# Kernel optimization log

Measured on AMD Instinct MI355X. Metric: run time of the kernel, lower is better.

The kernel has to match this reference:

```python
import jax, jax.numpy as jnp
import numpy as np

PAD = 1
VOCAB, D, HOPS = 32000, 256, 3

def _gru_dir(x_tbd, h0, Wih, Whh, bih, bhh):
    # x_tbd: [T,B,D]; PyTorch GRU gate math
    def step(h, xt):
        gx = xt @ Wih.T + bih            # [B,3D]
        gh = h @ Whh.T + bhh
        xr, xz, xn = jnp.split(gx, 3, axis=-1)
        hr, hz, hn = jnp.split(gh, 3, axis=-1)
        r = jax.nn.sigmoid(xr + hr)
        z = jax.nn.sigmoid(xz + hz)
        n = jnp.tanh(xn + r * hn)
        h2 = (1.0 - z) * n + z * h
        return h2, h2
    hT, ys = jax.lax.scan(step, h0, x_tbd)
    return ys, hT

def _embed_bag(table, idx):
    # idx: [B,L,M] -> sum over M -> [B,L,D]
    return jnp.take(table, idx, axis=0).sum(axis=2)

def _add_lm(full_mem, kb_len, conv_len, hiddens):
    # full_mem: [B,L,D]; hiddens: [B,T,D]; write hiddens into rows [kb, kb+cl)
    B, L, _ = full_mem.shape
    T = hiddens.shape[1]
    pos = jnp.arange(L)[None, :]                      # [1,L]
    rel = pos - kb_len[:, None]                        # [B,L]
    valid = (rel >= 0) & (rel < conv_len[:, None])
    rel_c = jnp.clip(rel, 0, T - 1)
    gathered = jnp.take_along_axis(hiddens, rel_c[:, :, None], axis=1)  # [B,L,D]
    return full_mem + jnp.where(valid[:, :, None], gathered, 0.0)

def setup_inputs() -> dict:
    key = jax.random.key(0)
    ks = jax.random.split(key, 20)
    B, T, L, M = 32, 128, 512, 4
    conv_seqs = jax.random.randint(ks[0], (B, T, M), 0, VOCAB)
    src_seqs = jax.random.randint(ks[1], (B, L, M), 0, VOCAB)
    kb_len = jnp.full((B,), L - T, dtype=jnp.int32)
    conv_len = jnp.full((B,), T, dtype=jnp.int32)
    def zero_pad(t):
        return t.at[PAD].set(0.0)
    emb_ctx = zero_pad(0.1 * jax.random.normal(ks[2], (VOCAB, D)))
    C_tables = zero_pad(0.1 * jax.random.normal(ks[3], (HOPS + 1, VOCAB, D)).transpose(1, 0, 2)).transpose(1, 0, 2)
    s = 1.0 / np.sqrt(D)
    Wih_f = jax.random.uniform(ks[4], (3 * D, D), minval=-s, maxval=s)
    Whh_f = jax.random.uniform(ks[5], (3 * D, D), minval=-s, maxval=s)
    bih_f = jax.random.uniform(ks[6], (3 * D,), minval=-s, maxval=s)
    bhh_f = jax.random.uniform(ks[7], (3 * D,), minval=-s, maxval=s)
    Wih_b = jax.random.uniform(ks[8], (3 * D, D), minval=-s, maxval=s)
    Whh_b = jax.random.uniform(ks[9], (3 * D, D), minval=-s, maxval=s)
    bih_b = jax.random.uniform(ks[10], (3 * D,), minval=-s, maxval=s)
    bhh_b = jax.random.uniform(ks[11], (3 * D,), minval=-s, maxval=s)
    W_w = jax.random.uniform(ks[12], (D, 2 * D), minval=-s, maxval=s)
    W_b = jax.random.uniform(ks[13], (D,), minval=-s, maxval=s)
    proj_w = jax.random.uniform(ks[14], (D, 2 * D), minval=-s, maxval=s)
    proj_b = jax.random.uniform(ks[15], (D,), minval=-s, maxval=s)
    return dict(conv_seqs=conv_seqs, src_seqs=src_seqs, kb_len=kb_len, conv_len=conv_len,
                emb_ctx=emb_ctx, C_tables=C_tables,
                Wih_f=Wih_f, Whh_f=Whh_f, bih_f=bih_f, bhh_f=bhh_f,
                Wih_b=Wih_b, Whh_b=Whh_b, bih_b=bih_b, bhh_b=bhh_b,
                W_w=W_w, W_b=W_b, proj_w=proj_w, proj_b=proj_b)

def reference(conv_seqs, src_seqs, kb_len, conv_len, emb_ctx, C_tables,
              Wih_f, Whh_f, bih_f, bhh_f, Wih_b, Whh_b, bih_b, bhh_b,
              W_w, W_b, proj_w, proj_b):
    B = conv_seqs.shape[0]
    # ContextRNN (dropout is identity at eval)
    emb = _embed_bag(emb_ctx, conv_seqs)               # [B,T,D]
    x = emb.transpose(1, 0, 2)                          # [T,B,D]
    h0 = jnp.zeros((B, D), emb.dtype)
    ys_f, hT_f = _gru_dir(x, h0, Wih_f, Whh_f, bih_f, bhh_f)
    ys_b, hT_b = _gru_dir(x[::-1], h0, Wih_b, Whh_b, bih_b, bhh_b)
    outputs = jnp.concatenate([ys_f, ys_b[::-1]], axis=-1).transpose(1, 0, 2)  # [B,T,2D]
    hidden = jnp.concatenate([hT_f, hT_b], axis=-1) @ W_w.T + W_b              # [B,D]
    rnn_out = outputs @ W_w.T + W_b                                            # [B,T,D]
    # ExternalKnowledge encode
    u = hidden
    prob_logit = None
    embed_C = None
    for hop in range(HOPS):
        embed_A = _add_lm(_embed_bag(C_tables[hop], src_seqs), kb_len, conv_len, rnn_out)
        embed_C = _add_lm(_embed_bag(C_tables[hop + 1], src_seqs), kb_len, conv_len, rnn_out)
        prob_logit = jnp.einsum('bld,bd->bl', embed_A, u)
        prob = jax.nn.softmax(prob_logit, axis=1)
        o_k = jnp.einsum('bld,bl->bd', embed_C, prob)
        u = u + o_k
    global_pointer = jax.nn.sigmoid(prob_logit)
    encoded = jax.nn.relu(jnp.concatenate([hidden, u], axis=-1) @ proj_w.T + proj_b)[None]
    return global_pointer, encoded
```

## Files before the change

### kernel.cpp

```cpp
#include <hip/hip_runtime.h>

typedef _Float16 f16;
typedef _Float16 f16x8 __attribute__((ext_vector_type(8)));
typedef _Float16 f16x4 __attribute__((ext_vector_type(4)));
typedef float    f32x4 __attribute__((ext_vector_type(4)));


__device__ __forceinline__ float frcp(float x){
  float r; asm("v_rcp_f32 %0, %1" : "=v"(r) : "v"(x)); return r;
}
__device__ __forceinline__ float fsig(float x){ return frcp(1.0f + __expf(-x)); }
__device__ __forceinline__ float ftanh(float x){ return 2.0f*frcp(1.0f + __expf(-2.0f*x)) - 1.0f; }

__global__ void k_zero(float* out){
  int i = blockIdx.x*256 + threadIdx.x;
  if (i < 24576) out[i] = 0.f;
}

__global__ void k_cvtall(const float* __restrict__ s0, const float* __restrict__ s1,
                         const float* __restrict__ s2, const float* __restrict__ s3,
                         const float* __restrict__ s4,
                         f16* __restrict__ d0, f16* __restrict__ d1,
                         f16* __restrict__ d2, f16* __restrict__ d3,
                         f16* __restrict__ d4){
  int i = blockIdx.x*256 + threadIdx.x;
  d0[i] = (f16)s0[i];
  d1[i] = (f16)s1[i];
  d2[i] = (f16)s2[i];
  d3[i] = (f16)s3[i];
  if (i < 131072) d4[i] = (f16)s4[i];
}

__global__ void k_embbag(const int* __restrict__ conv, const float* __restrict__ tbl,
                         f16* __restrict__ emb){
  int bt = blockIdx.x, d = threadIdx.x;
  const int* ix = conv + (size_t)bt*4;
  float s = 0.f;
#pragma unroll
  for (int m = 0; m < 4; ++m) s += tbl[(size_t)ix[m]*256 + d];
  emb[(size_t)bt*256 + d] = (f16)s;
}

__global__ __launch_bounds__(256) void k_gx(const f16* __restrict__ emb,
                                            const f16* __restrict__ W16,
                                            const float* __restrict__ bih,
                                            const float* __restrict__ bhh,
                                            f16* __restrict__ gx, int rev){
  int lane = threadIdx.x & 63, wv = threadIdx.x >> 6;
  int l16 = lane & 15, l4 = lane >> 4;
  int mrow = blockIdx.x*64 + wv*16;
  int m = mrow + l16;
  int t = m >> 5, b = m & 31;
  int tsrc = rev ? (127 - t) : t;
  const f16* arow = emb + (size_t)(b*128 + tsrc)*256;
  f16x8 af[8];
#pragma unroll
  for (int kt = 0; kt < 8; ++kt) af[kt] = *(const f16x8*)(arow + kt*32 + l4*8);

  for (int nt = 0; nt < 48; ++nt){
    int n = nt*16 + l16;
    const f16* brow = W16 + (size_t)n*256;
    f32x4 acc = {0.f,0.f,0.f,0.f};
#pragma unroll
    for (int kt = 0; kt < 8; ++kt){
      f16x8 bf = *(const f16x8*)(brow + kt*32 + l4*8);
      acc = __builtin_amdgcn_mfma_f32_16x16x32_f16(af[kt], bf, acc, 0, 0, 0);
    }
    float bias = bih[n] + (n < 512 ? bhh[n] : 0.f);
#pragma unroll
    for (int r = 0; r < 4; ++r){
      int m2 = mrow + l4*4 + r;
      gx[(size_t)m2*768 + n] = (f16)(acc[r] + bias);
    }
  }
}

__global__ __launch_bounds__(512, 1) void k_gru(const f16* __restrict__ gx_f,
                                                const f16* __restrict__ gx_b,
                                                const f16* __restrict__ whhf16,
                                                const f16* __restrict__ whhb16,
                                                const float* __restrict__ bhh_f,
                                                const float* __restrict__ bhh_b,
                                                f16* __restrict__ Abuf){
  int dir = blockIdx.x >> 1, grp = blockIdx.x & 1, b0 = grp*16;
  const f16*   gx  = dir ? gx_b   : gx_f;
  const f16*   Whh = dir ? whhb16 : whhf16;
  const float* bhh = dir ? bhh_b  : bhh_f;

  int tid = threadIdx.x, lane = tid & 63, wv = tid >> 6;
  int l16 = lane & 15, l4 = lane >> 4;

  __shared__ __align__(16) f16   a16[2][16][264];
  __shared__ __align__(16) float bhnL[256];
  for (int i = tid; i < (16*264*2)/4; i += 512) ((unsigned*)&a16[0][0][0])[i] = 0u;
  if (tid < 256) bhnL[tid] = bhh[512 + tid];

  f16x8 aW[2][3][8];
#pragma unroll
  for (int q = 0; q < 2; ++q){
    int Q = 2*wv + q;
#pragma unroll
    for (int g = 0; g < 3; ++g){
      const f16* wrow = Whh + (size_t)(g*256 + Q*16 + l16)*256;
#pragma unroll
      for (int kt = 0; kt < 8; ++kt) aW[q][g][kt] = *(const f16x8*)(wrow + kt*32 + l4*8);
    }
  }

  const f16* gp = gx + (size_t)(b0 + l16)*768;
  f16* ap  = Abuf + (size_t)(b0 + l16)*128*512 + dir*256 + (size_t)(dir ? 127 : 0)*512;
  int  astep = dir ? -512 : 512;
  f16* app = ap;

  const int d00 = (2*wv    )*16 + l4*4;
  const int d01 = (2*wv + 1)*16 + l4*4;

  f16x4 pend[2];
  pend[0] = (f16x4){(f16)0.f,(f16)0.f,(f16)0.f,(f16)0.f};
  pend[1] = (f16x4){(f16)0.f,(f16)0.f,(f16)0.f,(f16)0.f};

  __syncthreads();

#pragma unroll 1
  for (int t = 0; t < 128; ++t){
    if (t){
      *(f16x4*)(app + d00) = pend[0];
      *(f16x4*)(app + d01) = pend[1];
    }
    f16x4 xg[2][3];
#pragma unroll
    for (int q = 0; q < 2; ++q)
#pragma unroll
      for (int g = 0; g < 3; ++g)
        xg[q][g] = *(const f16x4*)(gp + g*256 + (2*wv+q)*16 + l4*4);

    const f16* rb = &a16[t & 1][l16][l4*8];

    f32x4 accr[2], accz[2];
#pragma unroll
    for (int q = 0; q < 2; ++q){ accr[q] = (f32x4){0.f,0.f,0.f,0.f};
                                 accz[q] = (f32x4){0.f,0.f,0.f,0.f}; }
#pragma unroll
    for (int kt = 0; kt < 8; ++kt){
      f16x8 bf = *(const f16x8*)(rb + kt*32);
#pragma unroll
      for (int q = 0; q < 2; ++q){
        accr[q] = __builtin_amdgcn_mfma_f32_16x16x32_f16(aW[q][0][kt], bf, accr[q], 0, 0, 0);
        accz[q] = __builtin_amdgcn_mfma_f32_16x16x32_f16(aW[q][1][kt], bf, accz[q], 0, 0, 0);
      }
    }
    f32x4 accn[2];
#pragma unroll
    for (int q = 0; q < 2; ++q) accn[q] = (f32x4){0.f,0.f,0.f,0.f};
#pragma unroll
    for (int kt = 0; kt < 8; ++kt){
      f16x8 bf = *(const f16x8*)(rb + kt*32);
#pragma unroll
      for (int q = 0; q < 2; ++q)
        accn[q] = __builtin_amdgcn_mfma_f32_16x16x32_f16(aW[q][2][kt], bf, accn[q], 0, 0, 0);
    }
    float rr[2][4], zz[2][4];
#pragma unroll
    for (int q = 0; q < 2; ++q)
#pragma unroll
      for (int r = 0; r < 4; ++r){
        rr[q][r] = fsig((float)xg[q][0][r] + accr[q][r]);
        zz[q][r] = fsig((float)xg[q][1][r] + accz[q][r]);
      }
    int nxt = (t & 1) ^ 1;
#pragma unroll
    for (int q = 0; q < 2; ++q){
      int d0 = (2*wv+q)*16 + l4*4;
      float4 bh4 = *(const float4*)(&bhnL[d0]);
      f16x4 hold = pend[q];
      f16x4 o4;
#pragma unroll
      for (int r = 0; r < 4; ++r){
        float bh = (r==0)?bh4.x:(r==1)?bh4.y:(r==2)?bh4.z:bh4.w;
        float nn = ftanh((float)xg[q][2][r] + rr[q][r]*(accn[q][r] + bh));
        float h2 = nn + zz[q][r]*((float)hold[r] - nn);
        o4[r] = (f16)h2;
      }
      *(f16x4*)(&a16[nxt][l16][d0]) = o4;
      pend[q] = o4;
    }
    app = ap; ap += astep;
    gp += 24576;
    __syncthreads();
  }
  *(f16x4*)(app + d00) = pend[0];
  *(f16x4*)(app + d01) = pend[1];
}

__global__ __launch_bounds__(256) void k_rnnout(const f16* __restrict__ Abuf,
                                                const f16* __restrict__ Ww16,
                                                const float* __restrict__ Wb,
                                                float* __restrict__ rnn){
  int lane = threadIdx.x & 63, wv = threadIdx.x >> 6;
  int l16 = lane & 15, l4 = lane >> 4;
  int mrow = blockIdx.x*64 + wv*16;
  const f16* arow = Abuf + (size_t)(mrow + l16)*512;
  f16x8 af[16];
#pragma unroll
  for (int kt = 0; kt < 16; ++kt) af[kt] = *(const f16x8*)(arow + kt*32 + l4*8);
  for (int nt = 0; nt < 16; ++nt){
    int n = nt*16 + l16;
    const f16* brow = Ww16 + (size_t)n*512;
    f32x4 acc = {0.f,0.f,0.f,0.f};
#pragma unroll
    for (int kt = 0; kt < 16; ++kt){
      f16x8 bf = *(const f16x8*)(brow + kt*32 + l4*8);
      acc = __builtin_amdgcn_mfma_f32_16x16x32_f16(af[kt], bf, acc, 0, 0, 0);
    }
    float bias = Wb[n];
#pragma unroll
    for (int r = 0; r < 4; ++r)
      rnn[(size_t)(mrow + l4*4 + r)*256 + n] = acc[r] + bias;
  }
}

__global__ __launch_bounds__(256) void k_hidden(const f16* __restrict__ Abuf,
                                                const f16* __restrict__ Ww16,
                                                const float* __restrict__ Wb,
                                                float* __restrict__ hidden,
                                                float* __restrict__ u){
  int lane = threadIdx.x & 63, wv = threadIdx.x >> 6;
  int l16 = lane & 15, l4 = lane >> 4;
  int mt = wv & 1, nt = blockIdx.x*2 + (wv >> 1);
  int b = mt*16 + l16;
  const f16* rowf = Abuf + ((size_t)b*128 + 127)*512;
  const f16* rowb = Abuf + ((size_t)b*128)*512;
  f16x8 af[16];
#pragma unroll
  for (int kt = 0; kt < 16; ++kt){
    int k = kt*32 + l4*8;
    af[kt] = *(const f16x8*)((k < 256 ? rowf : rowb) + k);
  }
  int n = nt*16 + l16;
  const f16* brow = Ww16 + (size_t)n*512;
  f32x4 acc = {0.f,0.f,0.f,0.f};
#pragma unroll
  for (int kt = 0; kt < 16; ++kt){
    f16x8 bf = *(const f16x8*)(brow + kt*32 + l4*8);
    acc = __builtin_amdgcn_mfma_f32_16x16x32_f16(af[kt], bf, acc, 0, 0, 0);
  }
  float bias = Wb[n];
#pragma unroll
  for (int r = 0; r < 4; ++r){
    int bo = mt*16 + l4*4 + r;
    float v = acc[r] + bias;
    hidden[(size_t)bo*256 + n] = v;
    u[(size_t)bo*256 + n] = v;
  }
}

__global__ __launch_bounds__(256) void k_logits(const int* __restrict__ src,
                                                const int* __restrict__ kbl,
                                                const int* __restrict__ cvl,
                                                const float* __restrict__ tblA,
                                                const float* __restrict__ rnn,
                                                const float* __restrict__ u,
                                                float* __restrict__ logits,
                                                const f16* __restrict__ bagin){
  int b = blockIdx.x >> 5, chunk = blockIdx.x & 31;
  int lane = threadIdx.x & 63, wv = threadIdx.x >> 6;
  float4 uv = *(const float4*)(u + b*256 + lane*4);
  if (bagin){
#pragma unroll
    for (int i = 0; i < 4; ++i){
      int l = chunk*16 + wv*4 + i;
      f16x4 bv = *(const f16x4*)(bagin + ((size_t)b*512 + l)*256 + lane*4);
      float p = (float)bv[0]*uv.x + (float)bv[1]*uv.y
              + (float)bv[2]*uv.z + (float)bv[3]*uv.w;
#pragma unroll
      for (int off = 32; off >= 1; off >>= 1) p += __shfl_down(p, off);
      if (lane == 0) logits[(size_t)b*512 + l] = p;
    }
    return;
  }
  int kb = kbl[b], cl = cvl[b];
#pragma unroll
  for (int i = 0; i < 4; ++i){
    int l = chunk*16 + wv*4 + i;
    const int* sp = src + ((size_t)b*512 + l)*4;
    float b0 = 0.f, b1 = 0.f, b2 = 0.f, b3 = 0.f;
#pragma unroll
    for (int m = 0; m < 4; ++m){
      float4 wq = *(const float4*)(tblA + (size_t)sp[m]*256 + lane*4);
      b0 += wq.x; b1 += wq.y; b2 += wq.z; b3 += wq.w;
    }
    int rel = l - kb;
    if (rel >= 0 && rel < cl){
      int rc = rel < 127 ? rel : 127;
      float4 rv = *(const float4*)(rnn + ((size_t)b*128 + rc)*256 + lane*4);
      b0 += rv.x; b1 += rv.y; b2 += rv.z; b3 += rv.w;
    }
    float p = b0*uv.x + b1*uv.y + b2*uv.z + b3*uv.w;
#pragma unroll
    for (int off = 32; off >= 1; off >>= 1) p += __shfl_down(p, off);
    if (lane == 0) logits[(size_t)b*512 + l] = p;
  }
}

__global__ __launch_bounds__(256) void k_okv(const int* __restrict__ src,
                                             const int* __restrict__ kbl,
                                             const int* __restrict__ cvl,
                                             const float* __restrict__ tblC,
                                             const float* __restrict__ rnn,
                                             const float* __restrict__ logits,
                                             float* __restrict__ u,
                                             float* __restrict__ gp_out, int write_gp,
                                             f16* __restrict__ bagout){
  int b = blockIdx.x >> 4, c = blockIdx.x & 15;
  int d = threadIdx.x, lane = d & 63, wv = d >> 6;
  __shared__ float red[4];
  __shared__ float bc;
  __shared__ float pr[512];
  __shared__ int   sidx[128];

  float v0 = logits[(size_t)b*512 + d];
  float v1 = logits[(size_t)b*512 + 256 + d];
  float m = fmaxf(v0, v1);
#pragma unroll
  for (int off = 32; off >= 1; off >>= 1) m = fmaxf(m, __shfl_down(m, off));
  if (lane == 0) red[wv] = m;
  __syncthreads();
  if (d == 0) bc = fmaxf(fmaxf(red[0], red[1]), fmaxf(red[2], red[3]));
  __syncthreads();
  float mx = bc;
  float e0 = __expf(v0 - mx), e1 = __expf(v1 - mx);
  float s = e0 + e1;
#pragma unroll
  for (int off = 32; off >= 1; off >>= 1) s += __shfl_down(s, off);
  __syncthreads();
  if (lane == 0) red[wv] = s;
  __syncthreads();
  if (d == 0) bc = red[0] + red[1] + red[2] + red[3];
  __syncthreads();
  float inv = 1.0f/bc;
  pr[d] = e0*inv; pr[256 + d] = e1*inv;
  if (d < 128) sidx[d] = src[(size_t)b*2048 + c*128 + d];
  if (write_gp && c == 0){
    gp_out[(size_t)b*512 + d]       = fsig(v0);
    gp_out[(size_t)b*512 + 256 + d] = fsig(v1);
  }
  __syncthreads();

  int kb = kbl[b], cl = cvl[b];
  float acc = 0.f;
  for (int l = 0; l < 32; ++l){
    const int* sp = sidx + l*4;
    float bag = tblC[(size_t)sp[0]*256 + d] + tblC[(size_t)sp[1]*256 + d]
              + tblC[(size_t)sp[2]*256 + d] + tblC[(size_t)sp[3]*256 + d];
    int rel = (c*32 + l) - kb;
    if (rel >= 0 && rel < cl){
      int rc = rel < 127 ? rel : 127;
      bag += rnn[((size_t)b*128 + rc)*256 + d];
    }
    if (bagout) bagout[((size_t)b*512 + c*32 + l)*256 + d] = (f16)bag;
    acc += pr[c*32 + l] * bag;
  }
  atomicAdd(&u[(size_t)b*256 + d], acc);
}

__global__ void k_encoded(const float* __restrict__ hidden, const float* __restrict__ u,
                          const float* __restrict__ pw, const float* __restrict__ pb,
                          float* __restrict__ out){
  int b = blockIdx.x, d = threadIdx.x;
  const float* w = pw + (size_t)d*512;
  float s = pb[d];
  for (int k = 0; k < 256; ++k) s += hidden[b*256 + k] * w[k];
  for (int k = 0; k < 256; ++k) s += u[b*256 + k]      * w[256 + k];
  out[(size_t)b*256 + d] = fmaxf(s, 0.f);
}

extern "C" void kernel_launch(void* const* d_in, const int* in_sizes, int n_in,
                              void* d_out, int out_size, void* d_ws, size_t ws_size,
                              hipStream_t stream){
  (void)in_sizes; (void)n_in; (void)out_size;
  float* out = (float*)d_out;

  const size_t WS_NEEDED = 25034752;
  if (ws_size < WS_NEEDED){
    k_zero<<<96, 256, 0, stream>>>(out);
    return;
  }

  const int* conv  = (const int*)d_in[0];
  const int* src   = (const int*)d_in[1];
  const int* kbl   = (const int*)d_in[2];
  const int* cvl   = (const int*)d_in[3];
  const float* emb_ctx = (const float*)d_in[4];
  const float* Ct      = (const float*)d_in[5];
  const float* Wih_f = (const float*)d_in[6];
  const float* Whh_f = (const float*)d_in[7];
  const float* bih_f = (const float*)d_in[8];
  const float* bhh_f = (const float*)d_in[9];
  const float* Wih_b = (const float*)d_in[10];
  const float* Whh_b = (const float*)d_in[11];
  const float* bih_b = (const float*)d_in[12];
  const float* bhh_b = (const float*)d_in[13];
  const float* Ww = (const float*)d_in[14];
  const float* Wb = (const float*)d_in[15];
  const float* pw = (const float*)d_in[16];
  const float* pb = (const float*)d_in[17];

  char* ws = (char*)d_ws;
  f16*   emb    = (f16*)(ws);
  f16*   gx_f   = (f16*)(ws + 2097152);
  f16*   gx_b   = (f16*)(ws + 8388608);
  f16*   Abuf   = (f16*)(ws + 14680064);
  float* rnn    = (float*)(ws + 18874368);
  float* hidden = (float*)(ws + 23068672);
  float* u      = (float*)(ws + 23101440);
  float* logits = (float*)(ws + 23134208);
  f16*   wihf16 = (f16*)(ws + 23199744);
  f16*   wihb16 = (f16*)(ws + 23592960);
  f16*   whhf16 = (f16*)(ws + 23986176);
  f16*   whhb16 = (f16*)(ws + 24379392);
  f16*   ww16   = (f16*)(ws + 24772608);
  f16*   bagbuf = (f16*)(ws + 2097152);

  k_cvtall<<<768, 256, 0, stream>>>(Wih_f, Wih_b, Whh_f, Whh_b, Ww,
                                    wihf16, wihb16, whhf16, whhb16, ww16);
  k_embbag<<<4096, 256, 0, stream>>>(conv, emb_ctx, emb);
  k_gx<<<64, 256, 0, stream>>>(emb, wihf16, bih_f, bhh_f, gx_f, 0);
  k_gx<<<64, 256, 0, stream>>>(emb, wihb16, bih_b, bhh_b, gx_b, 1);
  k_gru<<<4, 512, 0, stream>>>(gx_f, gx_b, whhf16, whhb16, bhh_f, bhh_b, Abuf);
  k_rnnout<<<64, 256, 0, stream>>>(Abuf, ww16, Wb, rnn);
  k_hidden<<<8, 256, 0, stream>>>(Abuf, ww16, Wb, hidden, u);

  for (int hop = 0; hop < 3; ++hop){
    const float* tA = Ct + (size_t)hop     * 32000 * 256;
    const float* tC = Ct + (size_t)(hop+1) * 32000 * 256;
    k_logits<<<1024, 256, 0, stream>>>(src, kbl, cvl, tA, rnn, u, logits,
                                       hop ? bagbuf : (const f16*)nullptr);
    k_okv<<<512, 256, 0, stream>>>(src, kbl, cvl, tC, rnn, logits, u,
                                   out, hop == 2 ? 1 : 0,
                                   hop < 2 ? bagbuf : (f16*)nullptr);
  }
  k_encoded<<<32, 256, 0, stream>>>(hidden, u, pw, pb, out + 16384);
}
```

Measured before the change: 848.5 us.

## Overlap hop embedding-bag gathers with GRU recurrence and merge small kernels

Extra blocks launched alongside the 4-block GRU kernel precompute the summed embedding bags for all C tables into spare workspace as fp16. The memory hops then read these bags instead of re-gathering four table rows per position. Several small launches are also merged (conversion with embedding, both gx directions, rnn-out with hidden). This uses the idle CUs during the serial recurrence, at the cost of extra workspace and possible contention with the GRU blocks.

```diff
diff --git a/kernel.cpp b/kernel.cpp
--- a/kernel.cpp
+++ b/kernel.cpp
@@ -17,23 +17,28 @@
   if (i < 24576) out[i] = 0.f;
 }
 
-__global__ void k_cvtall(const float* __restrict__ s0, const float* __restrict__ s1,
-                         const float* __restrict__ s2, const float* __restrict__ s3,
-                         const float* __restrict__ s4,
-                         f16* __restrict__ d0, f16* __restrict__ d1,
-                         f16* __restrict__ d2, f16* __restrict__ d3,
-                         f16* __restrict__ d4){
-  int i = blockIdx.x*256 + threadIdx.x;
-  d0[i] = (f16)s0[i];
-  d1[i] = (f16)s1[i];
-  d2[i] = (f16)s2[i];
-  d3[i] = (f16)s3[i];
-  if (i < 131072) d4[i] = (f16)s4[i];
-}
-
-__global__ void k_embbag(const int* __restrict__ conv, const float* __restrict__ tbl,
-                         f16* __restrict__ emb){
-  int bt = blockIdx.x, d = threadIdx.x;
+__global__ __launch_bounds__(256) void k_prep(const float* __restrict__ s0,
+                                              const float* __restrict__ s1,
+                                              const float* __restrict__ s2,
+                                              const float* __restrict__ s3,
+                                              const float* __restrict__ s4,
+                                              f16* __restrict__ d0, f16* __restrict__ d1,
+                                              f16* __restrict__ d2, f16* __restrict__ d3,
+                                              f16* __restrict__ d4,
+                                              const int* __restrict__ conv,
+                                              const float* __restrict__ tbl,
+                                              f16* __restrict__ emb){
+  int bid = blockIdx.x;
+  if (bid < 768){
+    int i = bid*256 + threadIdx.x;
+    d0[i] = (f16)s0[i];
+    d1[i] = (f16)s1[i];
+    d2[i] = (f16)s2[i];
+    d3[i] = (f16)s3[i];
+    if (i < 131072) d4[i] = (f16)s4[i];
+    return;
+  }
+  int bt = bid - 768, d = threadIdx.x;
   const int* ix = conv + (size_t)bt*4;
   float s = 0.f;
 #pragma unroll
@@ -41,14 +46,24 @@
   emb[(size_t)bt*256 + d] = (f16)s;
 }
 
-__global__ __launch_bounds__(256) void k_gx(const f16* __restrict__ emb,
-                                            const f16* __restrict__ W16,
-                                            const float* __restrict__ bih,
-                                            const float* __restrict__ bhh,
-                                            f16* __restrict__ gx, int rev){
+__global__ __launch_bounds__(256) void k_gx2(const f16* __restrict__ emb,
+                                             const f16* __restrict__ wf,
+                                             const f16* __restrict__ wb,
+                                             const float* __restrict__ bih_f,
+                                             const float* __restrict__ bhh_f,
+                                             const float* __restrict__ bih_b,
+                                             const float* __restrict__ bhh_b,
+                                             f16* __restrict__ gx_f,
+                                             f16* __restrict__ gx_b){
+  int rev = blockIdx.x >> 6, blk = blockIdx.x & 63;
+  const f16* W16 = rev ? wb : wf;
+  const float* bih = rev ? bih_b : bih_f;
+  const float* bhh = rev ? bhh_b : bhh_f;
+  f16* gx = rev ? gx_b : gx_f;
+
   int lane = threadIdx.x & 63, wv = threadIdx.x >> 6;
   int l16 = lane & 15, l4 = lane >> 4;
-  int mrow = blockIdx.x*64 + wv*16;
+  int mrow = blk*64 + wv*16;
   int m = mrow + l16;
   int t = m >> 5, b = m & 31;
   int tsrc = rev ? (127 - t) : t;
@@ -75,14 +90,39 @@
   }
 }
 
-__global__ __launch_bounds__(512, 1) void k_gru(const f16* __restrict__ gx_f,
-                                                const f16* __restrict__ gx_b,
-                                                const f16* __restrict__ whhf16,
-                                                const f16* __restrict__ whhb16,
-                                                const float* __restrict__ bhh_f,
-                                                const float* __restrict__ bhh_b,
-                                                f16* __restrict__ Abuf){
-  int dir = blockIdx.x >> 1, grp = blockIdx.x & 1, b0 = grp*16;
+__global__ __launch_bounds__(512, 1) void k_grumega(const f16* __restrict__ gx_f,
+                                                    const f16* __restrict__ gx_b,
+                                                    const f16* __restrict__ whhf16,
+                                                    const f16* __restrict__ whhb16,
+                                                    const float* __restrict__ bhh_f,
+                                                    const float* __restrict__ bhh_b,
+                                                    f16* __restrict__ Abuf,
+                                                    const int* __restrict__ src,
+                                                    const float* __restrict__ Ct,
+                                                    f16* __restrict__ bagT,
+                                                    int tab0, int tab1, int tab2, int tab3){
+  int bid = blockIdx.x;
+  if (bid >= 4){
+    int gi = bid - 4;
+    int slot = gi >> 6;
+    int tab = slot == 0 ? tab0 : slot == 1 ? tab1 : slot == 2 ? tab2 : tab3;
+    const float* tbl = Ct + (size_t)tab * 32000 * 256;
+    f16* dst = bagT + (size_t)slot * 4194304;
+    int tid = threadIdx.x;
+    int d = tid & 255, half = tid >> 8;
+    int base = (gi & 63) * 256;
+#pragma unroll 2
+    for (int it = 0; it < 128; ++it){
+      int task = base + it*2 + half;
+      int4 ix = *(const int4*)(src + (size_t)task*4);
+      float s = tbl[(size_t)ix.x*256 + d] + tbl[(size_t)ix.y*256 + d]
+              + tbl[(size_t)ix.z*256 + d] + tbl[(size_t)ix.w*256 + d];
+      dst[(size_t)task*256 + d] = (f16)s;
+    }
+    return;
+  }
+
+  int dir = bid >> 1, grp = bid & 1, b0 = grp*16;
   const f16*   gx  = dir ? gx_b   : gx_f;
   const f16*   Whh = dir ? whhb16 : whhf16;
   const float* bhh = dir ? bhh_b  : bhh_f;
@@ -192,41 +232,39 @@
   *(f16x4*)(app + d01) = pend[1];
 }
 
-__global__ __launch_bounds__(256) void k_rnnout(const f16* __restrict__ Abuf,
-                                                const f16* __restrict__ Ww16,
-                                                const float* __restrict__ Wb,
-                                                float* __restrict__ rnn){
+__global__ __launch_bounds__(256) void k_post(const f16* __restrict__ Abuf,
+                                              const f16* __restrict__ Ww16,
+                                              const float* __restrict__ Wb,
+                                              float* __restrict__ rnn,
+                                              float* __restrict__ hidden,
+                                              float* __restrict__ u){
+  int bid = blockIdx.x;
   int lane = threadIdx.x & 63, wv = threadIdx.x >> 6;
   int l16 = lane & 15, l4 = lane >> 4;
-  int mrow = blockIdx.x*64 + wv*16;
-  const f16* arow = Abuf + (size_t)(mrow + l16)*512;
-  f16x8 af[16];
-#pragma unroll
-  for (int kt = 0; kt < 16; ++kt) af[kt] = *(const f16x8*)(arow + kt*32 + l4*8);
-  for (int nt = 0; nt < 16; ++nt){
-    int n = nt*16 + l16;
-    const f16* brow = Ww16 + (size_t)n*512;
-    f32x4 acc = {0.f,0.f,0.f,0.f};
-#pragma unroll
-    for (int kt = 0; kt < 16; ++kt){
-      f16x8 bf = *(const f16x8*)(brow + kt*32 + l4*8);
-      acc = __builtin_amdgcn_mfma_f32_16x16x32_f16(af[kt], bf, acc, 0, 0, 0);
-    }
-    float bias = Wb[n];
-#pragma unroll
-    for (int r = 0; r < 4; ++r)
-      rnn[(size_t)(mrow + l4*4 + r)*256 + n] = acc[r] + bias;
-  }
-}
-
-__global__ __launch_bounds__(256) void k_hidden(const f16* __restrict__ Abuf,
-                                                const f16* __restrict__ Ww16,
-                                                const float* __restrict__ Wb,
-                                                float* __restrict__ hidden,
-                                                float* __restrict__ u){
-  int lane = threadIdx.x & 63, wv = threadIdx.x >> 6;
-  int l16 = lane & 15, l4 = lane >> 4;
-  int mt = wv & 1, nt = blockIdx.x*2 + (wv >> 1);
+  if (bid < 64){
+    int mrow = bid*64 + wv*16;
+    const f16* arow = Abuf + (size_t)(mrow + l16)*512;
+    f16x8 af[16];
+#pragma unroll
+    for (int kt = 0; kt < 16; ++kt) af[kt] = *(const f16x8*)(arow + kt*32 + l4*8);
+    for (int nt = 0; nt < 16; ++nt){
+      int n = nt*16 + l16;
+      const f16* brow = Ww16 + (size_t)n*512;
+      f32x4 acc = {0.f,0.f,0.f,0.f};
+#pragma unroll
+      for (int kt = 0; kt < 16; ++kt){
+        f16x8 bf = *(const f16x8*)(brow + kt*32 + l4*8);
+        acc = __builtin_amdgcn_mfma_f32_16x16x32_f16(af[kt], bf, acc, 0, 0, 0);
+      }
+      float bias = Wb[n];
+#pragma unroll
+      for (int r = 0; r < 4; ++r)
+        rnn[(size_t)(mrow + l4*4 + r)*256 + n] = acc[r] + bias;
+    }
+    return;
+  }
+  int hb = bid - 64;
+  int mt = wv & 1, nt = hb*2 + (wv >> 1);
   int b = mt*16 + l16;
   const f16* rowf = Abuf + ((size_t)b*128 + 127)*512;
   const f16* rowb = Abuf + ((size_t)b*128)*512;
@@ -261,33 +299,26 @@
                                                 const float* __restrict__ rnn,
                                                 const float* __restrict__ u,
                                                 float* __restrict__ logits,
-                                                const f16* __restrict__ bagin){
+                                                const f16* __restrict__ bag){
   int b = blockIdx.x >> 5, chunk = blockIdx.x & 31;
   int lane = threadIdx.x & 63, wv = threadIdx.x >> 6;
+  int kb = kbl[b], cl = cvl[b];
   float4 uv = *(const float4*)(u + b*256 + lane*4);
-  if (bagin){
-#pragma unroll
-    for (int i = 0; i < 4; ++i){
-      int l = chunk*16 + wv*4 + i;
-      f16x4 bv = *(const f16x4*)(bagin + ((size_t)b*512 + l)*256 + lane*4);
-      float p = (float)bv[0]*uv.x + (float)bv[1]*uv.y
-              + (float)bv[2]*uv.z + (float)bv[3]*uv.w;
-#pragma unroll
-      for (int off = 32; off >= 1; off >>= 1) p += __shfl_down(p, off);
-      if (lane == 0) logits[(size_t)b*512 + l] = p;
-    }
-    return;
-  }
-  int kb = kbl[b], cl = cvl[b];
 #pragma unroll
   for (int i = 0; i < 4; ++i){
     int l = chunk*16 + wv*4 + i;
-    const int* sp = src + ((size_t)b*512 + l)*4;
-    float b0 = 0.f, b1 = 0.f, b2 = 0.f, b3 = 0.f;
-#pragma unroll
-    for (int m = 0; m < 4; ++m){
-      float4 wq = *(const float4*)(tblA + (size_t)sp[m]*256 + lane*4);
-      b0 += wq.x; b1 += wq.y; b2 += wq.z; b3 += wq.w;
+    float b0, b1, b2, b3;
+    if (bag){
+      f16x4 bv = *(const f16x4*)(bag + ((size_t)b*512 + l)*256 + lane*4);
+      b0 = (float)bv[0]; b1 = (float)bv[1]; b2 = (float)bv[2]; b3 = (float)bv[3];
+    } else {
+      const int* sp = src + ((size_t)b*512 + l)*4;
+      b0 = b1 = b2 = b3 = 0.f;
+#pragma unroll
+      for (int m = 0; m < 4; ++m){
+        float4 wq = *(const float4*)(tblA + (size_t)sp[m]*256 + lane*4);
+        b0 += wq.x; b1 += wq.y; b2 += wq.z; b3 += wq.w;
+      }
     }
     int rel = l - kb;
     if (rel >= 0 && rel < cl){
@@ -310,6 +341,7 @@
                                              const float* __restrict__ logits,
                                              float* __restrict__ u,
                                              float* __restrict__ gp_out, int write_gp,
+                                             const f16* __restrict__ bagin,
                                              f16* __restrict__ bagout){
   int b = blockIdx.x >> 4, c = blockIdx.x & 15;
   int d = threadIdx.x, lane = d & 63, wv = d >> 6;
@@ -349,15 +381,20 @@
   int kb = kbl[b], cl = cvl[b];
   float acc = 0.f;
   for (int l = 0; l < 32; ++l){
-    const int* sp = sidx + l*4;
-    float bag = tblC[(size_t)sp[0]*256 + d] + tblC[(size_t)sp[1]*256 + d]
-              + tblC[(size_t)sp[2]*256 + d] + tblC[(size_t)sp[3]*256 + d];
+    float bag;
+    if (bagin){
+      bag = (float)bagin[((size_t)b*512 + c*32 + l)*256 + d];
+    } else {
+      const int* sp = sidx + l*4;
+      bag = tblC[(size_t)sp[0]*256 + d] + tblC[(size_t)sp[1]*256 + d]
+          + tblC[(size_t)sp[2]*256 + d] + tblC[(size_t)sp[3]*256 + d];
+      if (bagout) bagout[((size_t)b*512 + c*32 + l)*256 + d] = (f16)bag;
+    }
     int rel = (c*32 + l) - kb;
     if (rel >= 0 && rel < cl){
       int rc = rel < 127 ? rel : 127;
       bag += rnn[((size_t)b*128 + rc)*256 + d];
     }
-    if (bagout) bagout[((size_t)b*512 + c*32 + l)*256 + d] = (f16)bag;
     acc += pr[c*32 + l] * bag;
   }
   atomicAdd(&u[(size_t)b*256 + d], acc);
@@ -420,24 +457,33 @@
   f16*   whhb16 = (f16*)(ws + 24379392);
   f16*   ww16   = (f16*)(ws + 24772608);
   f16*   bagbuf = (f16*)(ws + 2097152);
-
-  k_cvtall<<<768, 256, 0, stream>>>(Wih_f, Wih_b, Whh_f, Whh_b, Ww,
-                                    wihf16, wihb16, whhf16, whhb16, ww16);
-  k_embbag<<<4096, 256, 0, stream>>>(conv, emb_ctx, emb);
-  k_gx<<<64, 256, 0, stream>>>(emb, wihf16, bih_f, bhh_f, gx_f, 0);
-  k_gx<<<64, 256, 0, stream>>>(emb, wihb16, bih_b, bhh_b, gx_b, 1);
-  k_gru<<<4, 512, 0, stream>>>(gx_f, gx_b, whhf16, whhb16, bhh_f, bhh_b, Abuf);
-  k_rnnout<<<64, 256, 0, stream>>>(Abuf, ww16, Wb, rnn);
-  k_hidden<<<8, 256, 0, stream>>>(Abuf, ww16, Wb, hidden, u);
+  f16*   bagT   = (f16*)(ws + WS_NEEDED);
+  size_t avail  = ws_size - WS_NEEDED;
+  int ntab = (int)(avail / 8388608); if (ntab > 4) ntab = 4;
+  const int tabids[4] = {1, 2, 3, 0};
+  const f16* bt[4] = {nullptr, nullptr, nullptr, nullptr};
+  for (int s = 0; s < ntab; ++s) bt[tabids[s]] = bagT + (size_t)s*4194304;
+
+  k_prep<<<4864, 256, 0, stream>>>(Wih_f, Wih_b, Whh_f, Whh_b, Ww,
+                                   wihf16, wihb16, whhf16, whhb16, ww16,
+                                   conv, emb_ctx, emb);
+  k_gx2<<<128, 256, 0, stream>>>(emb, wihf16, wihb16,
+                                 bih_f, bhh_f, bih_b, bhh_b, gx_f, gx_b);
+  k_grumega<<<4 + 64*ntab, 512, 0, stream>>>(gx_f, gx_b, whhf16, whhb16,
+                                             bhh_f, bhh_b, Abuf,
+                                             src, Ct, bagT,
+                                             tabids[0], tabids[1], tabids[2], tabids[3]);
+  k_post<<<72, 256, 0, stream>>>(Abuf, ww16, Wb, rnn, hidden, u);
 
   for (int hop = 0; hop < 3; ++hop){
     const float* tA = Ct + (size_t)hop     * 32000 * 256;
     const float* tC = Ct + (size_t)(hop+1) * 32000 * 256;
-    k_logits<<<1024, 256, 0, stream>>>(src, kbl, cvl, tA, rnn, u, logits,
-                                       hop ? bagbuf : (const f16*)nullptr);
+    const f16* lbag = bt[hop] ? bt[hop] : (hop ? bagbuf : (const f16*)nullptr);
+    const f16* obag = bt[hop + 1];
+    f16* obout = (!obag && hop < 2) ? bagbuf : (f16*)nullptr;
+    k_logits<<<1024, 256, 0, stream>>>(src, kbl, cvl, tA, rnn, u, logits, lbag);
     k_okv<<<512, 256, 0, stream>>>(src, kbl, cvl, tC, rnn, logits, u,
-                                   out, hop == 2 ? 1 : 0,
-                                   hop < 2 ? bagbuf : (f16*)nullptr);
+                                   out, hop == 2 ? 1 : 0, obag, obout);
   }
   k_encoded<<<32, 256, 0, stream>>>(hidden, u, pw, pb, out + 16384);
 }
```

Measured after the change: 745.3 us. -12.2%, faster.
